# Performance work log

Measured on AMD Instinct MI355X. Metric: run time of the kernel, lower is better.

The kernel has to match this reference:

```python
import jax, jax.numpy as jnp
import numpy as np

E = 1024
H = 16
D = E // H  # head_dim = 64
B, S = 8, 1024


def setup_inputs() -> dict:
    key = jax.random.key(0)
    ks = jax.random.split(key, 5)
    x = jax.random.normal(ks[0], (B, S, E), dtype=jnp.float32)
    # nn.Linear(E, 3E): weight [3E, E], bias [3E]
    w_in = jax.random.normal(ks[1], (3 * E, E), dtype=jnp.float32) * (1.0 / np.sqrt(E))
    b_in = jax.random.normal(ks[2], (3 * E,), dtype=jnp.float32) * 0.02
    # nn.Linear(E, E)
    w_out = jax.random.normal(ks[3], (E, E), dtype=jnp.float32) * (1.0 / np.sqrt(E))
    b_out = jax.random.normal(ks[4], (E,), dtype=jnp.float32) * 0.02
    return {"x": x, "w_in": w_in, "b_in": b_in, "w_out": w_out, "b_out": b_out}


def reference(x, w_in, b_in, w_out, b_out):
    Bb, Ss, _ = x.shape
    # fused QKV projection: x @ W.T + b -> [B, S, 3E]
    qkv = jnp.einsum('bse,fe->bsf', x, w_in) + b_in
    # reshape to [B, H, S, 3D] then split
    qkv = qkv.reshape(Bb, Ss, H, 3 * D).transpose(0, 2, 1, 3)
    q, k, v = jnp.split(qkv, 3, axis=-1)  # each [B, H, S, D]
    scale = 1.0 / jnp.sqrt(jnp.asarray(D, dtype=x.dtype))
    logits = jnp.einsum('bhqd,bhkd->bhqk', q, k) * scale  # [B, H, S, S]
    attn = jax.nn.softmax(logits, axis=-1)
    values = jnp.einsum('bhqk,bhkd->bhqd', attn, v)  # [B, H, S, D]
    values = values.transpose(0, 2, 1, 3).reshape(Bb, Ss, E)
    out = jnp.einsum('bse,fe->bsf', values, w_out) + b_out
    return out
```

## Files before the change

kernel.cpp:

```cpp
#include <hip/hip_runtime.h>

typedef short short8 __attribute__((ext_vector_type(8)));
typedef float f32x4 __attribute__((ext_vector_type(4)));

#define AS1 __attribute__((address_space(1)))
#define AS3 __attribute__((address_space(3)))

__device__ __forceinline__ void gload16(const void* g, void* l) {
    __builtin_amdgcn_global_load_lds((const AS1 unsigned int*)g, (AS3 unsigned int*)l, 16, 0, 0);
}

__device__ __forceinline__ unsigned short f2bf(float f) {
    union { float f; unsigned u; } c; c.f = f;
    unsigned r = (c.u + 0x7FFFu + ((c.u >> 16) & 1u)) >> 16;
    return (unsigned short)r;
}

__device__ __forceinline__ unsigned cvtpk(float a, float b) {
    unsigned r;
    asm("v_cvt_pk_bf16_f32 %0, %1, %2" : "=v"(r) : "v"(a), "v"(b));
    return r;
}

__device__ __forceinline__ void mfma16(f32x4& d, short8 a, short8 b) {
    asm("v_mfma_f32_16x16x32_bf16 %0, %1, %2, %0" : "+v"(d) : "v"(a), "v"(b));
}

#define QSCALE 0.18033688011112042f
#define SMREF 24.0f

#define XN4 2097152
#define WIN4 786432
#define WOUT4 262144
__global__ __launch_bounds__(256) void cvt_all(const float* __restrict__ x,
                                               const float* __restrict__ w_in,
                                               const float* __restrict__ w_out,
                                               unsigned short* __restrict__ xb,
                                               unsigned short* __restrict__ winb,
                                               unsigned short* __restrict__ woutb) {
    int idx = blockIdx.x * 256 + threadIdx.x;
    int stride = gridDim.x * 256;
    for (int i = idx; i < XN4 + WIN4 + WOUT4; i += stride) {
        const float4* src;
        ushort4* dst;
        int j;
        if (i < XN4) {
            src = (const float4*)x; dst = (ushort4*)xb; j = i;
        } else if (i < XN4 + WIN4) {
            src = (const float4*)w_in; dst = (ushort4*)winb; j = i - XN4;
        } else {
            src = (const float4*)w_out; dst = (ushort4*)woutb; j = i - XN4 - WIN4;
        }
        float4 v = src[j];
        ushort4 o;
        o.x = f2bf(v.x); o.y = f2bf(v.y); o.z = f2bf(v.z); o.w = f2bf(v.w);
        dst[j] = o;
    }
}

template <int EPI>
__global__ __launch_bounds__(256) void gemm_nt(
    const unsigned short* __restrict__ A, const unsigned short* __restrict__ B,
    const float* __restrict__ bias, int M, int N, int K,
    float* __restrict__ Cf, unsigned short* __restrict__ qb,
    unsigned short* __restrict__ kb, unsigned short* __restrict__ vtb) {
    __shared__ unsigned short As[128 * 64];
    __shared__ unsigned short Bs[128 * 64];
    const int tid = threadIdx.x;
    const int lane = tid & 63;
    const int wv = tid >> 6;
    const int wm = (wv >> 1) * 64, wn = (wv & 1) * 64;
    const int lr = lane & 15, lg = lane >> 4;
    const int x7 = lr & 7;
    const int m0 = blockIdx.x * 128, n0 = blockIdx.y * 128;

    f32x4 acc[4][4];
#pragma unroll
    for (int i = 0; i < 4; i++)
#pragma unroll
        for (int j = 0; j < 4; j++) acc[i][j] = (f32x4){0.f, 0.f, 0.f, 0.f};

    const int sr = tid >> 3;
    const int sc = ((tid & 7) ^ ((tid >> 3) & 7)) * 8;
    const unsigned short* Ag = A + (size_t)(m0 + sr) * K + sc;
    const unsigned short* Bg = B + (size_t)(n0 + sr) * K + sc;
    unsigned short* Asl = As + tid * 8;
    unsigned short* Bsl = Bs + tid * 8;

    for (int kt = 0; kt < K; kt += 64) {
        __syncthreads();
#pragma unroll
        for (int i = 0; i < 4; i++) {
            gload16(Ag + (size_t)(i * 32) * K + kt, Asl + i * 2048);
            gload16(Bg + (size_t)(i * 32) * K + kt, Bsl + i * 2048);
        }
        __syncthreads();
#pragma unroll
        for (int ks = 0; ks < 2; ks++) {
            short8 af[4], bf[4];
#pragma unroll
            for (int mi = 0; mi < 4; mi++)
                af[mi] = *(const short8*)(As + (wm + mi * 16 + lr) * 64 +
                                          (((ks * 4 + lg) ^ x7) * 8));
#pragma unroll
            for (int ni = 0; ni < 4; ni++)
                bf[ni] = *(const short8*)(Bs + (wn + ni * 16 + lr) * 64 +
                                          (((ks * 4 + lg) ^ x7) * 8));
            __builtin_amdgcn_s_setprio(1);
#pragma unroll
            for (int mi = 0; mi < 4; mi++)
#pragma unroll
                for (int ni = 0; ni < 4; ni++) mfma16(acc[mi][ni], af[mi], bf[ni]);
            __builtin_amdgcn_s_setprio(0);
        }
    }

#pragma unroll
    for (int ni = 0; ni < 4; ni++) {
        const int col = n0 + wn + ni * 16 + lr;
        const float bia = bias[col];
        const unsigned h = (unsigned)col / 192u;
        const int rem = col - (int)h * 192;
        const int tq = rem >> 6, d = rem & 63;
#pragma unroll
        for (int mi = 0; mi < 4; mi++) {
            const int row = m0 + wm + mi * 16 + lg * 4;
            if (EPI == 1) {
#pragma unroll
                for (int r = 0; r < 4; r++)
                    Cf[(size_t)(row + r) * N + col] = acc[mi][ni][r] + bia;
            } else {
                const int bb = row >> 10, s = row & 1023;
                const int bh = bb * 16 + (int)h;
                if (tq == 0) {
#pragma unroll
                    for (int r = 0; r < 4; r++)
                        qb[((size_t)bh * 1024 + s + r) * 64 + d] =
                            f2bf((acc[mi][ni][r] + bia) * QSCALE);
                } else if (tq == 1) {
#pragma unroll
                    for (int r = 0; r < 4; r++)
                        kb[((size_t)bh * 1024 + s + r) * 64 + d] = f2bf(acc[mi][ni][r] + bia);
                } else {
                    uint2 pk;
                    pk.x = cvtpk(acc[mi][ni][0] + bia, acc[mi][ni][1] + bia);
                    pk.y = cvtpk(acc[mi][ni][2] + bia, acc[mi][ni][3] + bia);
                    *(uint2*)(vtb + ((size_t)bh * 64 + d) * 1024 + s) = pk;
                }
            }
        }
    }
}

__device__ __forceinline__ void softmax_half(f32x4 (&s)[4], float& lpart,
                                             unsigned short* pbuf,
                                             int lr, int lg, int x7) {
    float p[4][4];
#pragma unroll
    for (int kt = 0; kt < 4; kt++)
#pragma unroll
        for (int r = 0; r < 4; r++) {
            p[kt][r] = __builtin_amdgcn_exp2f(s[kt][r] - SMREF);
            lpart += p[kt][r];
        }
#pragma unroll
    for (int kt = 0; kt < 4; kt++)
#pragma unroll
        for (int w2 = 0; w2 < 2; w2++) {
            const unsigned pk = cvtpk(p[kt][2 * w2], p[kt][2 * w2 + 1]);
            const int col = (kt * 16 + lg * 4 + 2 * w2) ^ (x7 << 3);
            *(unsigned*)(pbuf + lr * 64 + col) = pk;
        }
}

__global__ __launch_bounds__(256) void attn_fwd(
    const unsigned short* __restrict__ qg, const unsigned short* __restrict__ kg,
    const unsigned short* __restrict__ vtg, unsigned short* __restrict__ vals) {
    __shared__ unsigned short Ks[2][64 * 64];
    __shared__ unsigned short Vts[2][64 * 64];
    __shared__ unsigned short Ps[4 * 2048];
    const int tid = threadIdx.x, lane = tid & 63, w = tid >> 6;
    const int lr = lane & 15, lg = lane >> 4;
    const int x7 = lr & 7;
    const int bh = blockIdx.x;
    const int q0 = blockIdx.y * 128 + w * 32;

    const unsigned short* qrowA = qg + ((size_t)bh * 1024 + q0 + lr) * 64;
    const unsigned short* qrowB = qrowA + 16 * 64;
    short8 qA[2], qB[2];
    qA[0] = *(const short8*)(qrowA + lg * 8);
    qA[1] = *(const short8*)(qrowA + 32 + lg * 8);
    qB[0] = *(const short8*)(qrowB + lg * 8);
    qB[1] = *(const short8*)(qrowB + 32 + lg * 8);

    f32x4 oA[4], oB[4];
    float lA = 0.f, lB = 0.f;
#pragma unroll
    for (int i = 0; i < 4; i++) {
        oA[i] = (f32x4){0.f, 0.f, 0.f, 0.f};
        oB[i] = (f32x4){0.f, 0.f, 0.f, 0.f};
    }

    const unsigned short* kb = kg + (size_t)bh * 65536;
    const unsigned short* vb = vtg + (size_t)bh * 65536;
    unsigned short* pwl = Ps + w * 2048;

    const int srow = tid >> 3;
    const int scol = ((tid & 7) ^ (srow & 7)) * 8;

    auto stage = [&](int kv0, int buf) {
#pragma unroll
        for (int i = 0; i < 2; i++) {
            gload16(kb + (size_t)(kv0 + i * 32 + srow) * 64 + scol,
                    &Ks[buf][i * 2048 + tid * 8]);
            gload16(vb + (size_t)(i * 32 + srow) * 1024 + kv0 + scol,
                    &Vts[buf][i * 2048 + tid * 8]);
        }
    };

    stage(0, 0);
    __syncthreads();

    for (int t = 0; t < 16; ++t) {
        const int buf = t & 1;
        if (t < 15) stage((t + 1) * 64, buf ^ 1);
        const unsigned short* Kb = Ks[buf];
        const unsigned short* Vb = Vts[buf];

        f32x4 sA[4], sB[4];
#pragma unroll
        for (int i = 0; i < 4; i++) {
            sA[i] = (f32x4){0.f, 0.f, 0.f, 0.f};
            sB[i] = (f32x4){0.f, 0.f, 0.f, 0.f};
        }
#pragma unroll
        for (int kt = 0; kt < 4; kt++) {
            const short8 k0 = *(const short8*)(Kb + (kt * 16 + lr) * 64 + ((0 + lg) ^ x7) * 8);
            const short8 k1 = *(const short8*)(Kb + (kt * 16 + lr) * 64 + ((4 + lg) ^ x7) * 8);
            __builtin_amdgcn_s_setprio(1);
            mfma16(sA[kt], k0, qA[0]);
            mfma16(sB[kt], k0, qB[0]);
            mfma16(sA[kt], k1, qA[1]);
            mfma16(sB[kt], k1, qB[1]);
            __builtin_amdgcn_s_setprio(0);
        }

        softmax_half(sA, lA, pwl, lr, lg, x7);
        softmax_half(sB, lB, pwl + 1024, lr, lg, x7);

        short8 pA[2], pB[2];
#pragma unroll
        for (int ks2 = 0; ks2 < 2; ks2++) {
            pA[ks2] = *(const short8*)(pwl + lr * 64 + (((ks2 * 4 + lg) ^ x7) * 8));
            pB[ks2] = *(const short8*)(pwl + 1024 + lr * 64 + (((ks2 * 4 + lg) ^ x7) * 8));
        }
#pragma unroll
        for (int mi = 0; mi < 4; mi++) {
            const short8 v0 = *(const short8*)(Vb + (mi * 16 + lr) * 64 + ((0 + lg) ^ x7) * 8);
            const short8 v1 = *(const short8*)(Vb + (mi * 16 + lr) * 64 + ((4 + lg) ^ x7) * 8);
            __builtin_amdgcn_s_setprio(1);
            mfma16(oA[mi], v0, pA[0]);
            mfma16(oB[mi], v0, pB[0]);
            mfma16(oA[mi], v1, pA[1]);
            mfma16(oB[mi], v1, pB[1]);
            __builtin_amdgcn_s_setprio(0);
        }

        __syncthreads();
    }

    lA += __shfl_xor(lA, 16); lA += __shfl_xor(lA, 32);
    lB += __shfl_xor(lB, 16); lB += __shfl_xor(lB, 32);

    const int bb = bh >> 4, hh = bh & 15;
    {
        const float inv = 1.f / lA;
        unsigned short* vp = vals + (size_t)(bb * 1024 + q0 + lr) * 1024 + hh * 64 + lg * 4;
#pragma unroll
        for (int mi = 0; mi < 4; mi++) {
            uint2 st;
            st.x = cvtpk(oA[mi][0] * inv, oA[mi][1] * inv);
            st.y = cvtpk(oA[mi][2] * inv, oA[mi][3] * inv);
            *(uint2*)(vp + mi * 16) = st;
        }
    }
    {
        const float inv = 1.f / lB;
        unsigned short* vp = vals + (size_t)(bb * 1024 + q0 + 16 + lr) * 1024 + hh * 64 + lg * 4;
#pragma unroll
        for (int mi = 0; mi < 4; mi++) {
            uint2 st;
            st.x = cvtpk(oB[mi][0] * inv, oB[mi][1] * inv);
            st.y = cvtpk(oB[mi][2] * inv, oB[mi][3] * inv);
            *(uint2*)(vp + mi * 16) = st;
        }
    }
}

extern "C" void kernel_launch(void* const* d_in, const int* in_sizes, int n_in,
                              void* d_out, int out_size, void* d_ws, size_t ws_size,
                              hipStream_t stream) {
    const float* x = (const float*)d_in[0];
    const float* w_in = (const float*)d_in[1];
    const float* b_in = (const float*)d_in[2];
    const float* w_out = (const float*)d_in[3];
    const float* b_out = (const float*)d_in[4];
    float* out = (float*)d_out;

    unsigned short* ws = (unsigned short*)d_ws;
    unsigned short* xb = ws;
    unsigned short* winb = xb + 8388608;
    unsigned short* woutb = winb + 3145728;
    unsigned short* qb = woutb + 1048576;
    unsigned short* kb = qb + 8388608;
    unsigned short* vtb = kb + 8388608;
    unsigned short* vals = xb;

    cvt_all<<<2048, 256, 0, stream>>>(x, w_in, w_out, xb, winb, woutb);

    gemm_nt<0><<<dim3(64, 24), 256, 0, stream>>>(xb, winb, b_in, 8192, 3072, 1024,
                                                 nullptr, qb, kb, vtb);
    attn_fwd<<<dim3(128, 8), 256, 0, stream>>>(qb, kb, vtb, vals);
    gemm_nt<1><<<dim3(64, 8), 256, 0, stream>>>(vals, woutb, b_out, 8192, 1024, 1024,
                                                out, nullptr, nullptr, nullptr);
}
```

Before: 148.5 us.

## Use 256x128 block tile for QKV projection GEMM with wider per-wave tiles

New measurement: 157.7 us. 6.2% more time.

```diff
diff --git a/kernel.cpp b/kernel.cpp
--- a/kernel.cpp
+++ b/kernel.cpp
@@ -58,12 +58,95 @@
     }
 }
 
-template <int EPI>
-__global__ __launch_bounds__(256) void gemm_nt(
+__global__ __launch_bounds__(256, 2) void gemm_qkv(
     const unsigned short* __restrict__ A, const unsigned short* __restrict__ B,
-    const float* __restrict__ bias, int M, int N, int K,
-    float* __restrict__ Cf, unsigned short* __restrict__ qb,
-    unsigned short* __restrict__ kb, unsigned short* __restrict__ vtb) {
+    const float* __restrict__ bias, int K,
+    unsigned short* __restrict__ qb, unsigned short* __restrict__ kb,
+    unsigned short* __restrict__ vtb) {
+    __shared__ unsigned short As[256 * 64];
+    __shared__ unsigned short Bs[128 * 64];
+    const int tid = threadIdx.x;
+    const int lane = tid & 63;
+    const int wv = tid >> 6;
+    const int lr = lane & 15, lg = lane >> 4;
+    const int x7 = lr & 7;
+    const int m0 = blockIdx.x * 256, n0 = blockIdx.y * 128;
+
+    f32x4 acc[4][8];
+#pragma unroll
+    for (int i = 0; i < 4; i++)
+#pragma unroll
+        for (int j = 0; j < 8; j++) acc[i][j] = (f32x4){0.f, 0.f, 0.f, 0.f};
+
+    const int sr = tid >> 3;
+    const int sc = ((tid & 7) ^ ((tid >> 3) & 7)) * 8;
+    const unsigned short* Ag = A + (size_t)(m0 + sr) * K + sc;
+    const unsigned short* Bg = B + (size_t)(n0 + sr) * K + sc;
+    unsigned short* Asl = As + tid * 8;
+    unsigned short* Bsl = Bs + tid * 8;
+
+    for (int kt = 0; kt < K; kt += 64) {
+        __syncthreads();
+#pragma unroll
+        for (int i = 0; i < 8; i++)
+            gload16(Ag + (size_t)(i * 32) * K + kt, Asl + i * 2048);
+#pragma unroll
+        for (int i = 0; i < 4; i++)
+            gload16(Bg + (size_t)(i * 32) * K + kt, Bsl + i * 2048);
+        __syncthreads();
+#pragma unroll
+        for (int ks = 0; ks < 2; ks++) {
+            const int co = ((ks * 4 + lg) ^ x7) * 8;
+            short8 af[4], bf[8];
+#pragma unroll
+            for (int mi = 0; mi < 4; mi++)
+                af[mi] = *(const short8*)(As + (wv * 64 + mi * 16 + lr) * 64 + co);
+#pragma unroll
+            for (int ni = 0; ni < 8; ni++)
+                bf[ni] = *(const short8*)(Bs + (ni * 16 + lr) * 64 + co);
+            __builtin_amdgcn_s_setprio(1);
+#pragma unroll
+            for (int mi = 0; mi < 4; mi++)
+#pragma unroll
+                for (int ni = 0; ni < 8; ni++) mfma16(acc[mi][ni], af[mi], bf[ni]);
+            __builtin_amdgcn_s_setprio(0);
+        }
+    }
+
+#pragma unroll
+    for (int ni = 0; ni < 8; ni++) {
+        const int col = n0 + ni * 16 + lr;
+        const float bia = bias[col];
+        const unsigned h = (unsigned)col / 192u;
+        const int rem = col - (int)h * 192;
+        const int tq = rem >> 6, d = rem & 63;
+#pragma unroll
+        for (int mi = 0; mi < 4; mi++) {
+            const int row = m0 + wv * 64 + mi * 16 + lg * 4;
+            const int bb = row >> 10, s = row & 1023;
+            const int bh = bb * 16 + (int)h;
+            if (tq == 0) {
+#pragma unroll
+                for (int r = 0; r < 4; r++)
+                    qb[((size_t)bh * 1024 + s + r) * 64 + d] =
+                        f2bf((acc[mi][ni][r] + bia) * QSCALE);
+            } else if (tq == 1) {
+#pragma unroll
+                for (int r = 0; r < 4; r++)
+                    kb[((size_t)bh * 1024 + s + r) * 64 + d] = f2bf(acc[mi][ni][r] + bia);
+            } else {
+                uint2 pk;
+                pk.x = cvtpk(acc[mi][ni][0] + bia, acc[mi][ni][1] + bia);
+                pk.y = cvtpk(acc[mi][ni][2] + bia, acc[mi][ni][3] + bia);
+                *(uint2*)(vtb + ((size_t)bh * 64 + d) * 1024 + s) = pk;
+            }
+        }
+    }
+}
+
+__global__ __launch_bounds__(256) void gemm_proj(
+    const unsigned short* __restrict__ A, const unsigned short* __restrict__ B,
+    const float* __restrict__ bias, int K, int N, float* __restrict__ Cf) {
     __shared__ unsigned short As[128 * 64];
     __shared__ unsigned short Bs[128 * 64];
     const int tid = threadIdx.x;
@@ -119,35 +202,12 @@
     for (int ni = 0; ni < 4; ni++) {
         const int col = n0 + wn + ni * 16 + lr;
         const float bia = bias[col];
-        const unsigned h = (unsigned)col / 192u;
-        const int rem = col - (int)h * 192;
-        const int tq = rem >> 6, d = rem & 63;
 #pragma unroll
         for (int mi = 0; mi < 4; mi++) {
             const int row = m0 + wm + mi * 16 + lg * 4;
-            if (EPI == 1) {
-#pragma unroll
-                for (int r = 0; r < 4; r++)
-                    Cf[(size_t)(row + r) * N + col] = acc[mi][ni][r] + bia;
-            } else {
-                const int bb = row >> 10, s = row & 1023;
-                const int bh = bb * 16 + (int)h;
-                if (tq == 0) {
-#pragma unroll
-                    for (int r = 0; r < 4; r++)
-                        qb[((size_t)bh * 1024 + s + r) * 64 + d] =
-                            f2bf((acc[mi][ni][r] + bia) * QSCALE);
-                } else if (tq == 1) {
-#pragma unroll
-                    for (int r = 0; r < 4; r++)
-                        kb[((size_t)bh * 1024 + s + r) * 64 + d] = f2bf(acc[mi][ni][r] + bia);
-                } else {
-                    uint2 pk;
-                    pk.x = cvtpk(acc[mi][ni][0] + bia, acc[mi][ni][1] + bia);
-                    pk.y = cvtpk(acc[mi][ni][2] + bia, acc[mi][ni][3] + bia);
-                    *(uint2*)(vtb + ((size_t)bh * 64 + d) * 1024 + s) = pk;
-                }
-            }
+#pragma unroll
+            for (int r = 0; r < 4; r++)
+                Cf[(size_t)(row + r) * N + col] = acc[mi][ni][r] + bia;
         }
     }
 }
@@ -318,9 +378,7 @@
 
     cvt_all<<<2048, 256, 0, stream>>>(x, w_in, w_out, xb, winb, woutb);
 
-    gemm_nt<0><<<dim3(64, 24), 256, 0, stream>>>(xb, winb, b_in, 8192, 3072, 1024,
-                                                 nullptr, qb, kb, vtb);
+    gemm_qkv<<<dim3(32, 24), 256, 0, stream>>>(xb, winb, b_in, 1024, qb, kb, vtb);
     attn_fwd<<<dim3(128, 8), 256, 0, stream>>>(qb, kb, vtb, vals);
-    gemm_nt<1><<<dim3(64, 8), 256, 0, stream>>>(vals, woutb, b_out, 8192, 1024, 1024,
-                                                out, nullptr, nullptr, nullptr);
-}
+    gemm_proj<<<dim3(64, 8), 256, 0, stream>>>(vals, woutb, b_out, 1024, 1024, out);
+}
```
